# Kernel optimization log

Hardware: AMD Instinct MI355X
Metric: run time of the kernel (lower is better)

The kernel has to match this reference:

```python
import jax, jax.numpy as jnp
import numpy as np

N_HEAD = 8
D_MODEL = 512
D_QKV = 64
LN_EPS = 1e-6


def setup_inputs() -> dict:
    key = jax.random.key(0)
    ks = jax.random.split(key, 10)
    B, S = 4, 2048
    q = jax.random.normal(ks[0], (B, S, D_MODEL), dtype=jnp.float32)
    k = jax.random.normal(ks[1], (B, S, D_MODEL), dtype=jnp.float32)
    v = jax.random.normal(ks[2], (B, S, D_MODEL), dtype=jnp.float32)
    mask = jax.random.randint(ks[3], (B, S, S), 0, 2, dtype=jnp.int32)
    scale = 1.0 / np.sqrt(D_MODEL)
    Wq = jax.random.normal(ks[4], (D_MODEL, N_HEAD * D_QKV), dtype=jnp.float32) * scale
    Wk = jax.random.normal(ks[5], (D_MODEL, N_HEAD * D_QKV), dtype=jnp.float32) * scale
    Wv = jax.random.normal(ks[6], (D_MODEL, N_HEAD * D_QKV), dtype=jnp.float32) * scale
    Wfc = jax.random.normal(ks[7], (N_HEAD * D_QKV, D_MODEL), dtype=jnp.float32) * scale
    gamma = jnp.ones((D_MODEL,), dtype=jnp.float32)
    beta = jnp.zeros((D_MODEL,), dtype=jnp.float32)
    return {"q": q, "k": k, "v": v, "mask": mask, "Wq": Wq, "Wk": Wk,
            "Wv": Wv, "Wfc": Wfc, "gamma": gamma, "beta": beta}


def _layer_norm(x, gamma, beta):
    mu = jnp.mean(x, axis=-1, keepdims=True)
    var = jnp.mean(jnp.square(x - mu), axis=-1, keepdims=True)
    return (x - mu) * jax.lax.rsqrt(var + LN_EPS) * gamma + beta


def reference(q, k, v, mask, Wq, Wk, Wv, Wfc, gamma, beta):
    B, Sq, _ = q.shape
    Sk = k.shape[1]
    residual = q
    qn = _layer_norm(q, gamma, beta)
    # projections -> [B, S, H, Dk]
    qh = (qn @ Wq).reshape(B, Sq, N_HEAD, D_QKV)
    kh = (k @ Wk).reshape(B, Sk, N_HEAD, D_QKV)
    vh = (v @ Wv).reshape(B, Sk, N_HEAD, D_QKV)
    temp = jnp.float32(D_QKV ** 0.5)
    # scores: [B, H, Sq, Sk]
    attn = jnp.einsum('bqhd,bkhd->bhqk', qh / temp, kh)
    attn = jnp.where(mask[:, None, :, :] == 0, jnp.float32(-1e9), attn)
    attn = jax.nn.softmax(attn, axis=-1)
    out = jnp.einsum('bhqk,bkhd->bqhd', attn, vh).reshape(B, Sq, N_HEAD * D_QKV)
    out = out @ Wfc
    return out + residual
```

## Files before the change

kernel.cpp:

```cpp
#include <hip/hip_runtime.h>

#define BATCH 4
#define SEQ   2048
#define NHEAD 8
#define DQKV  64
#define DMODEL 512
#define ROWS  (BATCH*SEQ)
#define BH    (BATCH*NHEAD)
#define HSTRIDE (SEQ*DQKV)

using f32x4  = __attribute__((ext_vector_type(4))) float;
using short8 = __attribute__((ext_vector_type(8))) short;
using short4v = __attribute__((ext_vector_type(4))) short;

#define MFMA16(a,b,c) __builtin_amdgcn_mfma_f32_16x16x32_bf16((a),(b),(c),0,0,0)

__device__ __forceinline__ short f2bf(float f) {
    unsigned u = __float_as_uint(f);
    u += 0x7FFFu + ((u >> 16) & 1u);
    return (short)(u >> 16);
}

__device__ __forceinline__ void gl2lds16(const short* g, short* l) {
    __builtin_amdgcn_global_load_lds(
        (__attribute__((address_space(1))) void*)g,
        (__attribute__((address_space(3))) void*)l, 16, 0, 0);
}

__device__ __forceinline__ void stage64x64(const short* g0, int gstride, short* lt, int t) {
    #pragma unroll
    for (int p = 0; p < 2; ++p) {
        int o = p * 2048 + t * 8;
        int row = o >> 6;
        int c = ((o >> 3) & 7) ^ (row & 7);
        gl2lds16(g0 + (size_t)row * gstride + c * 8, lt + o);
    }
}
__device__ __forceinline__ void stage128x64(const short* g0, int gstride, short* lt, int t) {
    stage64x64(g0, gstride, lt, t);
    stage64x64(g0 + (size_t)64 * gstride, gstride, lt + 4096, t);
}

__device__ __forceinline__ short8 trd(const short* t, int row, int c) {
    return *(const short8*)(t + row * 64 + ((c ^ (row & 7)) << 3));
}

__global__ __launch_bounds__(256) void prep_kernel(
        const float* __restrict__ q, const float* __restrict__ k,
        const float* __restrict__ v, const float* __restrict__ gamma,
        const float* __restrict__ beta,
        short* __restrict__ qn, short* __restrict__ kb, short* __restrict__ vb) {
    if (blockIdx.y == 0) {
        int wave = threadIdx.x >> 6, lane = threadIdx.x & 63;
        int row  = blockIdx.x * 4 + wave;
        const float4* qr = (const float4*)(q + (size_t)row * DMODEL);
        float4 x0 = qr[lane * 2];
        float4 x1 = qr[lane * 2 + 1];
        float s  = x0.x + x0.y + x0.z + x0.w + x1.x + x1.y + x1.z + x1.w;
        float s2 = x0.x*x0.x + x0.y*x0.y + x0.z*x0.z + x0.w*x0.w
                 + x1.x*x1.x + x1.y*x1.y + x1.z*x1.z + x1.w*x1.w;
        #pragma unroll
        for (int m = 1; m < 64; m <<= 1) {
            s  += __shfl_xor(s,  m);
            s2 += __shfl_xor(s2, m);
        }
        float mu  = s * (1.0f / DMODEL);
        float var = s2 * (1.0f / DMODEL) - mu * mu;
        float rstd = rsqrtf(var + 1e-6f);
        const float4* g = (const float4*)gamma;
        const float4* be = (const float4*)beta;
        float4 g0 = g[lane*2], g1 = g[lane*2+1];
        float4 b0 = be[lane*2], b1 = be[lane*2+1];
        short8 o;
        o[0] = f2bf((x0.x - mu) * rstd * g0.x + b0.x);
        o[1] = f2bf((x0.y - mu) * rstd * g0.y + b0.y);
        o[2] = f2bf((x0.z - mu) * rstd * g0.z + b0.z);
        o[3] = f2bf((x0.w - mu) * rstd * g0.w + b0.w);
        o[4] = f2bf((x1.x - mu) * rstd * g1.x + b1.x);
        o[5] = f2bf((x1.y - mu) * rstd * g1.y + b1.y);
        o[6] = f2bf((x1.z - mu) * rstd * g1.z + b1.z);
        o[7] = f2bf((x1.w - mu) * rstd * g1.w + b1.w);
        ((short8*)(qn + (size_t)row * DMODEL))[lane] = o;
    } else {
        const float* src = (blockIdx.y == 1) ? k : v;
        short* dst = (blockIdx.y == 1) ? kb : vb;
        size_t i = (size_t)blockIdx.x * 2048 + (size_t)threadIdx.x * 8;
        float4 a = *(const float4*)(src + i);
        float4 b = *(const float4*)(src + i + 4);
        short8 o;
        o[0]=f2bf(a.x); o[1]=f2bf(a.y); o[2]=f2bf(a.z); o[3]=f2bf(a.w);
        o[4]=f2bf(b.x); o[5]=f2bf(b.y); o[6]=f2bf(b.z); o[7]=f2bf(b.w);
        *(short8*)(dst + i) = o;
    }
}

__global__ __launch_bounds__(256) void castWT4_kernel(
        const float* __restrict__ W0, const float* __restrict__ W1,
        const float* __restrict__ W2, const float* __restrict__ W3,
        short* __restrict__ T0, short* __restrict__ T1,
        short* __restrict__ T2, short* __restrict__ T3) {
    __shared__ short tile[64 * 68];
    int w = blockIdx.z;
    const float* W = w==0 ? W0 : w==1 ? W1 : w==2 ? W2 : W3;
    short* T = w==0 ? T0 : w==1 ? T1 : w==2 ? T2 : T3;
    int ti = blockIdx.x, tj = blockIdx.y;
    int tid = threadIdx.x;
    #pragma unroll
    for (int p = 0; p < 4; ++p) {
        int idx = tid + p * 256;
        int kl = idx >> 4, c4 = idx & 15;
        float4 f = *(const float4*)(W + (size_t)(tj*64 + kl) * DMODEL + ti*64 + c4*4);
        short4v s; s[0]=f2bf(f.x); s[1]=f2bf(f.y); s[2]=f2bf(f.z); s[3]=f2bf(f.w);
        *(short4v*)(tile + kl*68 + c4*4) = s;
    }
    __syncthreads();
    #pragma unroll
    for (int p = 0; p < 4; ++p) {
        int idx = tid + p * 256;
        int nl = idx >> 4, kseg = idx & 15;
        short4v s;
        #pragma unroll
        for (int i = 0; i < 4; ++i) s[i] = tile[(kseg*4 + i)*68 + nl];
        *(short4v*)(T + (size_t)(ti*64 + nl) * DMODEL + tj*64 + kseg*4) = s;
    }
}

__global__ __launch_bounds__(256) void maskpack_kernel(
        const int* __restrict__ mask, unsigned long long* __restrict__ mp) {
    int gw = blockIdx.x * 4 + (threadIdx.x >> 6);
    int lane = threadIdx.x & 63;
    int r   = gw & 3;
    int rg  = (gw >> 2) & 1;
    int w64 = (gw >> 3) & 31;
    int qg  = (gw >> 8) & 63;
    int b   = gw >> 14;
    int row = qg * 32 + rg * 16 + (lane >> 4) * 4 + r;
    const int* src = mask + ((size_t)b * SEQ + row) * SEQ + w64 * 64 + (lane & 15);
    unsigned long long w0 = __ballot(src[0]  != 0);
    unsigned long long w1 = __ballot(src[16] != 0);
    unsigned long long w2 = __ballot(src[32] != 0);
    unsigned long long w3 = __ballot(src[48] != 0);
    if (lane == 0) {
        unsigned long long* d = mp + (size_t)gw * 4;
        d[0] = w0; d[1] = w1; d[2] = w2; d[3] = w3;
    }
}

__global__ __launch_bounds__(256, 4) void proj_qkv_kernel(
        const short* __restrict__ qn, const short* __restrict__ kb,
        const short* __restrict__ vb,
        const short* __restrict__ Wqt, const short* __restrict__ Wkt,
        const short* __restrict__ Wvt,
        short* __restrict__ qhp, short* __restrict__ khp, short* __restrict__ vtp) {
    __shared__ __align__(16) short Wl[2 * 8192];
    int tid = threadIdx.x, wave = tid >> 6, lane = tid & 63;
    int lm = lane & 15, lg = lane >> 4;
    int which = blockIdx.y >> 2;
    int CB0 = (blockIdx.y & 3) * 128;
    const short* A  = which==0 ? qn  : which==1 ? kb  : vb;
    const short* Wt = which==0 ? Wqt : which==1 ? Wkt : Wvt;
    float scale = which==0 ? 0.18033688f : 1.0f;

    int RBw = blockIdx.x * 128 + wave * 32;
    const short* Arow0 = A + (size_t)(RBw + lm) * DMODEL;
    const short* Arow1 = A + (size_t)(RBw + 16 + lm) * DMODEL;
    const short* W0 = Wt + (size_t)CB0 * DMODEL;

    short8 a[2][2];
    a[0][0] = *(const short8*)(Arow0 + lg * 8);
    a[0][1] = *(const short8*)(Arow0 + 32 + lg * 8);
    a[1][0] = *(const short8*)(Arow1 + lg * 8);
    a[1][1] = *(const short8*)(Arow1 + 32 + lg * 8);
    stage128x64(W0, DMODEL, Wl, tid);
    __syncthreads();

    f32x4 acc[2][8] = {};
    for (int kk = 0; kk < DMODEL; kk += 64) {
        int cur = (kk >> 6) & 1;
        bool more = (kk + 64) < DMODEL;
        short8 an[2][2];
        if (more) {
            stage128x64(W0 + kk + 64, DMODEL, Wl + (cur ^ 1) * 8192, tid);
            an[0][0] = *(const short8*)(Arow0 + kk + 64 + lg * 8);
            an[0][1] = *(const short8*)(Arow0 + kk + 96 + lg * 8);
            an[1][0] = *(const short8*)(Arow1 + kk + 64 + lg * 8);
            an[1][1] = *(const short8*)(Arow1 + kk + 96 + lg * 8);
        }
        const short* Wc = Wl + cur * 8192;
        #pragma unroll
        for (int cg = 0; cg < 8; ++cg) {
            short8 b0 = trd(Wc, cg*16 + lm, lg);
            short8 b1 = trd(Wc, cg*16 + lm, lg + 4);
            #pragma unroll
            for (int rg = 0; rg < 2; ++rg) {
                acc[rg][cg] = MFMA16(a[rg][0], b0, acc[rg][cg]);
                acc[rg][cg] = MFMA16(a[rg][1], b1, acc[rg][cg]);
            }
        }
        if (more) {
            #pragma unroll
            for (int rg = 0; rg < 2; ++rg) { a[rg][0] = an[rg][0]; a[rg][1] = an[rg][1]; }
        }
        __syncthreads();
    }

    if (which < 2) {
        short* outh = which==0 ? qhp : khp;
        #pragma unroll
        for (int rg = 0; rg < 2; ++rg) {
            #pragma unroll
            for (int cg = 0; cg < 8; ++cg) {
                int n = CB0 + cg * 16 + lm;
                int h = n >> 6, d = n & 63;
                #pragma unroll
                for (int r = 0; r < 4; ++r) {
                    int m = RBw + rg * 16 + lg * 4 + r;
                    int bb = m >> 11, s = m & 2047;
                    outh[(size_t)(bb * NHEAD + h) * HSTRIDE + (size_t)s * DQKV + d] =
                        f2bf(acc[rg][cg][r] * scale);
                }
            }
        }
    } else {
        int bb = RBw >> 11;
        #pragma unroll
        for (int rg = 0; rg < 2; ++rg) {
            int s0 = (RBw + rg * 16 + lg * 4) & 2047;
            #pragma unroll
            for (int cg = 0; cg < 8; ++cg) {
                int n = CB0 + cg * 16 + lm;
                int h = n >> 6, d = n & 63;
                short4v pk;
                #pragma unroll
                for (int r = 0; r < 4; ++r) pk[r] = f2bf(acc[rg][cg][r]);
                *(short4v*)(vtp + (size_t)(bb * NHEAD + h) * HSTRIDE
                            + (size_t)d * SEQ + s0) = pk;
            }
        }
    }
}

__global__ __launch_bounds__(256, 4) void attn_kernel(
        const short* __restrict__ qh, const short* __restrict__ kh,
        const short* __restrict__ vt, const unsigned long long* __restrict__ mpack,
        short* __restrict__ oh) {
    __shared__ __align__(16) short lds[20480];
    int tid = threadIdx.x, wave = tid >> 6, lane = tid & 63;
    int lm = lane & 15, lg = lane >> 4;
    int qt = blockIdx.x, bh = blockIdx.y, b = bh >> 3;
    int qbase = qt * 64 + wave * 16;
    short* Pw = lds + 16384 + wave * 1024;

    const short* Kbase = kh + (size_t)bh * HSTRIDE;
    const short* Vtb   = vt + (size_t)bh * HSTRIDE;

    const short8* Qrow = (const short8*)(qh + (size_t)bh * HSTRIDE
                          + (size_t)(qbase + lm) * DQKV);
    short8 aq0 = Qrow[lg];
    short8 aq1 = Qrow[lg + 4];

    int mblk = __builtin_amdgcn_readfirstlane(
        ((b * 64 + qt * 2 + (wave >> 1)) << 10) + ((wave & 1) << 4));
    const unsigned long long* mbase = mpack + mblk;

    const short one = (short)0x3F80;
    short8 ones = {one, one, one, one, one, one, one, one};

    f32x4 o[4] = {};
    f32x4 ox{};

    stage64x64(Kbase, DQKV, lds, tid);
    stage64x64(Vtb,   SEQ,  lds + 8192, tid);
    __syncthreads();

    for (int kt = 0; kt < SEQ; kt += 64) {
        int cur = (kt >> 6) & 1;
        if (kt + 64 < SEQ) {
            int nxt = cur ^ 1;
            stage64x64(Kbase + (size_t)(kt + 64) * DQKV, DQKV, lds + nxt * 4096, tid);
            stage64x64(Vtb + kt + 64, SEQ, lds + 8192 + nxt * 4096, tid);
        }
        const short* Kc = lds + cur * 4096;
        const short* Vc = lds + 8192 + cur * 4096;

        f32x4 sk[4];
        #pragma unroll
        for (int kg = 0; kg < 4; ++kg) {
            short8 bk0 = trd(Kc, kg*16 + lm, lg);
            short8 bk1 = trd(Kc, kg*16 + lm, lg + 4);
            f32x4 z{};
            z = MFMA16(aq0, bk0, z);
            sk[kg] = MFMA16(aq1, bk1, z);
        }

        const unsigned long long* mw = mbase + (kt >> 6) * 32;
        #pragma unroll
        for (int r = 0; r < 4; ++r) {
            int row = lg * 4 + r;
            short* pd = Pw + row * 64 + (lm & 7);
            #pragma unroll
            for (int kg = 0; kg < 4; ++kg) {
                unsigned long long mword = mw[r * 4 + kg];
                float e = __builtin_amdgcn_exp2f(sk[kg][r]);
                float pe;
                asm("v_cndmask_b32 %0, 0, %1, %2" : "=v"(pe) : "v"(e), "s"(mword));
                int c = (2 * kg + (lm >> 3)) ^ (row & 7);
                pd[c * 8] = f2bf(pe);
            }
        }

        short8 ap0 = trd(Pw, lm, lg);
        short8 ap1 = trd(Pw, lm, lg + 4);

        #pragma unroll
        for (int dt = 0; dt < 4; ++dt) {
            short8 bv0 = trd(Vc, dt*16 + lm, lg);
            short8 bv1 = trd(Vc, dt*16 + lm, lg + 4);
            o[dt] = MFMA16(ap0, bv0, o[dt]);
            o[dt] = MFMA16(ap1, bv1, o[dt]);
        }
        ox = MFMA16(ap0, ones, ox);
        ox = MFMA16(ap1, ones, ox);
        __syncthreads();
    }

    short* ob = oh + (size_t)bh * HSTRIDE;
    float rinv[4];
    #pragma unroll
    for (int r = 0; r < 4; ++r) rinv[r] = __builtin_amdgcn_rcpf(ox[r]);
    #pragma unroll
    for (int dt = 0; dt < 4; ++dt) {
        #pragma unroll
        for (int r = 0; r < 4; ++r) {
            ob[(size_t)(qbase + lg * 4 + r) * DQKV + dt * 16 + lm] =
                f2bf(o[dt][r] * rinv[r]);
        }
    }
}

__global__ __launch_bounds__(256, 4) void outproj_kernel(
        const short* __restrict__ Ah, const short* __restrict__ Wfct,
        const float* __restrict__ resid, float* __restrict__ out) {
    __shared__ __align__(16) short Wl[2 * 4096];
    int tid = threadIdx.x, wave = tid >> 6, lane = tid & 63;
    int lm = lane & 15, lg = lane >> 4;
    int CB0 = blockIdx.y * 64;
    int RB = blockIdx.x * 64 + wave * 16;
    const short* W0 = Wfct + (size_t)CB0 * DMODEL;

    int m0 = RB + lm;
    size_t rb = (size_t)(m0 >> 11) * (NHEAD * HSTRIDE) + (size_t)(m0 & 2047) * DQKV;

    short8 a0 = *(const short8*)(Ah + rb + lg * 8);
    short8 a1 = *(const short8*)(Ah + rb + 32 + lg * 8);
    stage64x64(W0, DMODEL, Wl, tid);
    __syncthreads();

    f32x4 acc[4] = {};
    for (int kk = 0; kk < DMODEL; kk += 64) {
        int cur = (kk >> 6) & 1;
        bool more = (kk + 64) < DMODEL;
        short8 a0n, a1n;
        if (more) {
            stage64x64(W0 + kk + 64, DMODEL, Wl + (cur ^ 1) * 4096, tid);
            size_t hoff = (size_t)((kk >> 6) + 1) * HSTRIDE;
            a0n = *(const short8*)(Ah + rb + hoff + lg * 8);
            a1n = *(const short8*)(Ah + rb + hoff + 32 + lg * 8);
        }
        const short* Wc = Wl + cur * 4096;
        #pragma unroll
        for (int cg = 0; cg < 4; ++cg) {
            short8 b0 = trd(Wc, cg*16 + lm, lg);
            short8 b1 = trd(Wc, cg*16 + lm, lg + 4);
            acc[cg] = MFMA16(a0, b0, acc[cg]);
            acc[cg] = MFMA16(a1, b1, acc[cg]);
        }
        if (more) { a0 = a0n; a1 = a1n; }
        __syncthreads();
    }

    #pragma unroll
    for (int cg = 0; cg < 4; ++cg) {
        int n = CB0 + cg * 16 + lm;
        #pragma unroll
        for (int r = 0; r < 4; ++r) {
            int m = RB + lg * 4 + r;
            size_t idx = (size_t)m * DMODEL + n;
            out[idx] = acc[cg][r] + resid[idx];
        }
    }
}

extern "C" void kernel_launch(void* const* d_in, const int* in_sizes, int n_in,
                              void* d_out, int out_size, void* d_ws, size_t ws_size,
                              hipStream_t stream) {
    const float* q     = (const float*)d_in[0];
    const float* k     = (const float*)d_in[1];
    const float* v     = (const float*)d_in[2];
    const int*   mask  = (const int*)d_in[3];
    const float* Wq    = (const float*)d_in[4];
    const float* Wk    = (const float*)d_in[5];
    const float* Wv    = (const float*)d_in[6];
    const float* Wfc   = (const float*)d_in[7];
    const float* gamma = (const float*)d_in[8];
    const float* beta  = (const float*)d_in[9];
    float* out = (float*)d_out;

    char* ws = (char*)d_ws;
    const size_t SZ_ROWS = (size_t)ROWS * DMODEL * sizeof(short);
    const size_t SZ_W    = (size_t)DMODEL * DMODEL * sizeof(short);
    short* qn   = (short*)(ws);
    short* kbf  = (short*)(ws + SZ_ROWS);
    short* vbf  = (short*)(ws + 2 * SZ_ROWS);
    short* Wqt  = (short*)(ws + 3 * SZ_ROWS);
    short* Wkt  = (short*)(ws + 3 * SZ_ROWS + SZ_W);
    short* Wvt  = (short*)(ws + 3 * SZ_ROWS + 2 * SZ_W);
    short* Wfct = (short*)(ws + 3 * SZ_ROWS + 3 * SZ_W);
    short* qhb  = (short*)(ws + 3 * SZ_ROWS + 4 * SZ_W);
    short* khb  = (short*)(ws + 4 * SZ_ROWS + 4 * SZ_W);
    short* vtb  = (short*)(ws + 5 * SZ_ROWS + 4 * SZ_W);
    unsigned long long* mpack = (unsigned long long*)(ws + 6 * SZ_ROWS + 4 * SZ_W);
    short* aout = qn;

    prep_kernel<<<dim3(ROWS / 4, 3), 256, 0, stream>>>(q, k, v, gamma, beta, qn, kbf, vbf);
    castWT4_kernel<<<dim3(8, 8, 4), 256, 0, stream>>>(Wq, Wk, Wv, Wfc, Wqt, Wkt, Wvt, Wfct);
    maskpack_kernel<<<65536 / 4, 256, 0, stream>>>(mask, mpack);

    proj_qkv_kernel<<<dim3(ROWS / 128, 12), 256, 0, stream>>>(
        qn, kbf, vbf, Wqt, Wkt, Wvt, qhb, khb, vtb);

    attn_kernel<<<dim3(SEQ / 64, BH), 256, 0, stream>>>(qhb, khb, vtb, mpack, aout);

    outproj_kernel<<<dim3(ROWS / 64, DMODEL / 64), 256, 0, stream>>>(aout, Wfct, q, out);
}
```

Baseline: 263.3 us.

## Double query rows per wave in attention and keep P in registers

Each attention block now covers 128 queries, with each wave handling two 16-row query groups against the same K/V tile, so each staged tile is reused twice. QK^T is computed transposed so the probabilities stay in registers and are packed with v_cvt_pk_bf16_f32, removing the LDS round-trip for P. The mask packing kernel uses vectorized int4 loads with a new layout, and blocks are remapped to interleave heads. Occupancy drops to 2 blocks per SM because register use rises.

```diff
diff --git a/kernel.cpp b/kernel.cpp
--- a/kernel.cpp
+++ b/kernel.cpp
@@ -43,6 +43,9 @@
 
 __device__ __forceinline__ short8 trd(const short* t, int row, int c) {
     return *(const short8*)(t + row * 64 + ((c ^ (row & 7)) << 3));
+}
+__device__ __forceinline__ short4v trd64(const short* t, int row, int chunk, int sub) {
+    return *(const short4v*)(t + row * 64 + ((chunk ^ (row & 7)) << 3) + sub * 4);
 }
 
 __global__ __launch_bounds__(256) void prep_kernel(
@@ -129,20 +132,23 @@
         const int* __restrict__ mask, unsigned long long* __restrict__ mp) {
     int gw = blockIdx.x * 4 + (threadIdx.x >> 6);
     int lane = threadIdx.x & 63;
-    int r   = gw & 3;
-    int rg  = (gw >> 2) & 1;
-    int w64 = (gw >> 3) & 31;
-    int qg  = (gw >> 8) & 63;
-    int b   = gw >> 14;
-    int row = qg * 32 + rg * 16 + (lane >> 4) * 4 + r;
-    const int* src = mask + ((size_t)b * SEQ + row) * SEQ + w64 * 64 + (lane & 15);
-    unsigned long long w0 = __ballot(src[0]  != 0);
-    unsigned long long w1 = __ballot(src[16] != 0);
-    unsigned long long w2 = __ballot(src[32] != 0);
-    unsigned long long w3 = __ballot(src[48] != 0);
-    if (lane == 0) {
-        unsigned long long* d = mp + (size_t)gw * 4;
-        d[0] = w0; d[1] = w1; d[2] = w2; d[3] = w3;
+    int lm = lane & 15, lg = lane >> 4;
+    int w64 = gw & 31;
+    int Qg  = (gw >> 5) & 127;
+    int b   = gw >> 12;
+    const int* src = mask + ((size_t)b * SEQ + Qg * 16 + lm) * SEQ + w64 * 64 + lg * 4;
+    unsigned long long* d = mp + (size_t)gw * 16;
+    #pragma unroll
+    for (int kg = 0; kg < 4; ++kg) {
+        int4 v = *(const int4*)(src + kg * 16);
+        unsigned long long w0 = __ballot(v.x != 0);
+        unsigned long long w1 = __ballot(v.y != 0);
+        unsigned long long w2 = __ballot(v.z != 0);
+        unsigned long long w3 = __ballot(v.w != 0);
+        if (lane == 0) {
+            *(ulonglong2*)(d + kg*4)     = make_ulonglong2(w0, w1);
+            *(ulonglong2*)(d + kg*4 + 2) = make_ulonglong2(w2, w3);
+        }
     }
 }
 
@@ -240,34 +246,38 @@
     }
 }
 
-__global__ __launch_bounds__(256, 4) void attn_kernel(
+__global__ __launch_bounds__(256, 2) void attn_kernel(
         const short* __restrict__ qh, const short* __restrict__ kh,
         const short* __restrict__ vt, const unsigned long long* __restrict__ mpack,
         short* __restrict__ oh) {
-    __shared__ __align__(16) short lds[20480];
+    __shared__ __align__(16) short lds[16384];
     int tid = threadIdx.x, wave = tid >> 6, lane = tid & 63;
     int lm = lane & 15, lg = lane >> 4;
-    int qt = blockIdx.x, bh = blockIdx.y, b = bh >> 3;
-    int qbase = qt * 64 + wave * 16;
-    short* Pw = lds + 16384 + wave * 1024;
+
+    int bid = blockIdx.y * gridDim.x + blockIdx.x;
+    int slot = bid >> 3;
+    int bh = (bid & 7) * 4 + (slot >> 4);
+    int qt = slot & 15;
+    int b = bh >> 3;
+    int qbase = qt * 128 + wave * 32;
 
     const short* Kbase = kh + (size_t)bh * HSTRIDE;
     const short* Vtb   = vt + (size_t)bh * HSTRIDE;
 
     const short8* Qrow = (const short8*)(qh + (size_t)bh * HSTRIDE
                           + (size_t)(qbase + lm) * DQKV);
-    short8 aq0 = Qrow[lg];
-    short8 aq1 = Qrow[lg + 4];
-
-    int mblk = __builtin_amdgcn_readfirstlane(
-        ((b * 64 + qt * 2 + (wave >> 1)) << 10) + ((wave & 1) << 4));
-    const unsigned long long* mbase = mpack + mblk;
+    short8 aq[2][2];
+    aq[0][0] = Qrow[lg];       aq[0][1] = Qrow[lg + 4];
+    aq[1][0] = Qrow[128 + lg]; aq[1][1] = Qrow[128 + lg + 4];
+
+    int mb = __builtin_amdgcn_readfirstlane((b * 128 + qt * 8 + wave * 2) * 512);
+    const unsigned long long* mbase = mpack + mb;
 
     const short one = (short)0x3F80;
-    short8 ones = {one, one, one, one, one, one, one, one};
-
-    f32x4 o[4] = {};
-    f32x4 ox{};
+    short8 ones8 = {one, one, one, one, one, one, one, one};
+
+    f32x4 o[2][4] = {};
+    f32x4 ox[2] = {};
 
     stage64x64(Kbase, DQKV, lds, tid);
     stage64x64(Vtb,   SEQ,  lds + 8192, tid);
@@ -282,58 +292,77 @@
         }
         const short* Kc = lds + cur * 4096;
         const short* Vc = lds + 8192 + cur * 4096;
-
-        f32x4 sk[4];
+        const unsigned long long* mw = mbase + (kt >> 6) * 16;
+
+        f32x4 sk[2][4];
         #pragma unroll
         for (int kg = 0; kg < 4; ++kg) {
-            short8 bk0 = trd(Kc, kg*16 + lm, lg);
-            short8 bk1 = trd(Kc, kg*16 + lm, lg + 4);
-            f32x4 z{};
-            z = MFMA16(aq0, bk0, z);
-            sk[kg] = MFMA16(aq1, bk1, z);
-        }
-
-        const unsigned long long* mw = mbase + (kt >> 6) * 32;
-        #pragma unroll
-        for (int r = 0; r < 4; ++r) {
-            int row = lg * 4 + r;
-            short* pd = Pw + row * 64 + (lm & 7);
-            #pragma unroll
-            for (int kg = 0; kg < 4; ++kg) {
-                unsigned long long mword = mw[r * 4 + kg];
-                float e = __builtin_amdgcn_exp2f(sk[kg][r]);
-                float pe;
-                asm("v_cndmask_b32 %0, 0, %1, %2" : "=v"(pe) : "v"(e), "s"(mword));
-                int c = (2 * kg + (lm >> 3)) ^ (row & 7);
-                pd[c * 8] = f2bf(pe);
-            }
-        }
-
-        short8 ap0 = trd(Pw, lm, lg);
-        short8 ap1 = trd(Pw, lm, lg + 4);
+            short8 ak0 = trd(Kc, kg * 16 + lm, lg);
+            short8 ak1 = trd(Kc, kg * 16 + lm, lg + 4);
+            #pragma unroll
+            for (int qg = 0; qg < 2; ++qg) {
+                f32x4 z{};
+                z = MFMA16(ak0, aq[qg][0], z);
+                sk[qg][kg] = MFMA16(ak1, aq[qg][1], z);
+            }
+        }
+
+        short8 pa8[2][2];
+        #pragma unroll
+        for (int qg = 0; qg < 2; ++qg) {
+            #pragma unroll
+            for (int kgp = 0; kgp < 2; ++kgp) {
+                float p[8];
+                #pragma unroll
+                for (int jj = 0; jj < 8; ++jj) {
+                    int kg = kgp * 2 + (jj >> 2), r = jj & 3;
+                    unsigned long long mword = mw[qg * 512 + kg * 4 + r];
+                    float e = __builtin_amdgcn_exp2f(sk[qg][kg][r]);
+                    asm("v_cndmask_b32 %0, 0, %1, %2" : "=v"(p[jj]) : "v"(e), "s"(mword));
+                }
+                int w0, w1, w2, w3;
+                asm("v_cvt_pk_bf16_f32 %0, %1, %2" : "=v"(w0) : "v"(p[0]), "v"(p[1]));
+                asm("v_cvt_pk_bf16_f32 %0, %1, %2" : "=v"(w1) : "v"(p[2]), "v"(p[3]));
+                asm("v_cvt_pk_bf16_f32 %0, %1, %2" : "=v"(w2) : "v"(p[4]), "v"(p[5]));
+                asm("v_cvt_pk_bf16_f32 %0, %1, %2" : "=v"(w3) : "v"(p[6]), "v"(p[7]));
+                union { int wi[4]; short8 s; } u;
+                u.wi[0] = w0; u.wi[1] = w1; u.wi[2] = w2; u.wi[3] = w3;
+                pa8[qg][kgp] = u.s;
+            }
+        }
 
         #pragma unroll
         for (int dt = 0; dt < 4; ++dt) {
-            short8 bv0 = trd(Vc, dt*16 + lm, lg);
-            short8 bv1 = trd(Vc, dt*16 + lm, lg + 4);
-            o[dt] = MFMA16(ap0, bv0, o[dt]);
-            o[dt] = MFMA16(ap1, bv1, o[dt]);
-        }
-        ox = MFMA16(ap0, ones, ox);
-        ox = MFMA16(ap1, ones, ox);
+            #pragma unroll
+            for (int kgp = 0; kgp < 2; ++kgp) {
+                short4v lo = trd64(Vc, dt * 16 + lm, kgp * 4 + (lg >> 1), lg & 1);
+                short4v hi = trd64(Vc, dt * 16 + lm, kgp * 4 + 2 + (lg >> 1), lg & 1);
+                short8 bv = __builtin_shufflevector(lo, hi, 0, 1, 2, 3, 4, 5, 6, 7);
+                o[0][dt] = MFMA16(pa8[0][kgp], bv, o[0][dt]);
+                o[1][dt] = MFMA16(pa8[1][kgp], bv, o[1][dt]);
+            }
+        }
+        #pragma unroll
+        for (int qg = 0; qg < 2; ++qg) {
+            ox[qg] = MFMA16(pa8[qg][0], ones8, ox[qg]);
+            ox[qg] = MFMA16(pa8[qg][1], ones8, ox[qg]);
+        }
         __syncthreads();
     }
 
     short* ob = oh + (size_t)bh * HSTRIDE;
-    float rinv[4];
-    #pragma unroll
-    for (int r = 0; r < 4; ++r) rinv[r] = __builtin_amdgcn_rcpf(ox[r]);
-    #pragma unroll
-    for (int dt = 0; dt < 4; ++dt) {
-        #pragma unroll
-        for (int r = 0; r < 4; ++r) {
-            ob[(size_t)(qbase + lg * 4 + r) * DQKV + dt * 16 + lm] =
-                f2bf(o[dt][r] * rinv[r]);
+    #pragma unroll
+    for (int qg = 0; qg < 2; ++qg) {
+        float rinv[4];
+        #pragma unroll
+        for (int r = 0; r < 4; ++r) rinv[r] = __builtin_amdgcn_rcpf(ox[qg][r]);
+        #pragma unroll
+        for (int dt = 0; dt < 4; ++dt) {
+            #pragma unroll
+            for (int r = 0; r < 4; ++r) {
+                ob[(size_t)(qbase + qg * 16 + lg * 4 + r) * DQKV + dt * 16 + lm] =
+                    f2bf(o[qg][dt][r] * rinv[r]);
+            }
         }
     }
 }
@@ -424,12 +453,12 @@
 
     prep_kernel<<<dim3(ROWS / 4, 3), 256, 0, stream>>>(q, k, v, gamma, beta, qn, kbf, vbf);
     castWT4_kernel<<<dim3(8, 8, 4), 256, 0, stream>>>(Wq, Wk, Wv, Wfc, Wqt, Wkt, Wvt, Wfct);
-    maskpack_kernel<<<65536 / 4, 256, 0, stream>>>(mask, mpack);
+    maskpack_kernel<<<16384 / 4, 256, 0, stream>>>(mask, mpack);
 
     proj_qkv_kernel<<<dim3(ROWS / 128, 12), 256, 0, stream>>>(
         qn, kbf, vbf, Wqt, Wkt, Wvt, qhb, khb, vtb);
 
-    attn_kernel<<<dim3(SEQ / 64, BH), 256, 0, stream>>>(qhb, khb, vtb, mpack, aout);
+    attn_kernel<<<dim3(SEQ / 128, BH), 256, 0, stream>>>(qhb, khb, vtb, mpack, aout);
 
     outproj_kernel<<<dim3(ROWS / 64, DMODEL / 64), 256, 0, stream>>>(aout, Wfct, q, out);
 }
```

New measurement: 260.6 us. No clear change (-1.0%).
